# Kernel optimization log

Measured on AMD Instinct MI355X. Metric: run time of the kernel, lower is better.

## Reference

```python
import jax, jax.numpy as jnp
import numpy as np

B, S, D = 4, 8192, 1024

def log_g(x):
    # log of g(x): log(x + 0.5) for x >= 0, log(sigmoid(x)) = -softplus(-x) otherwise
    return jnp.where(x >= 0, jnp.log(jax.nn.relu(x) + 0.5), -jax.nn.softplus(-x))

def setup_inputs() -> dict:
    key = jax.random.key(0)
    k1, k2 = jax.random.split(key)
    x = jax.random.normal(k1, (B, S, D), dtype=jnp.float32)
    # Linear(dim, 3*dim, bias=False); stored as [dim, 3*dim] so y = x @ W
    W = jax.random.normal(k2, (D, 3 * D), dtype=jnp.float32) * (1.0 / np.sqrt(D))
    return {"x": x, "W": W}

def reference(x, W):
    # x: [B, S, D], W: [D, 3D]
    hW = jnp.einsum('bsd,de->bse', x, W)  # [B, S, 3D]
    hidden, f_gate, i_gate = jnp.split(hW, 3, axis=-1)

    # log-space normalized gates:
    # diff = softplus(-f) - softplus(-i); log_f' = -softplus(diff); log_i' = -softplus(-diff)
    diff = jax.nn.softplus(-f_gate) - jax.nn.softplus(-i_gate)
    log_f = -jax.nn.softplus(diff)
    log_i = -jax.nn.softplus(-diff)
    log_values = log_i + log_g(hidden)

    # Heinsen associative scan in log space (float32 internally)
    a_star = jnp.cumsum(log_f.astype(jnp.float32), axis=1)
    log_h0_plus_b_star = jax.lax.cumlogsumexp(log_values.astype(jnp.float32) - a_star, axis=1)
    log_h = a_star + log_h0_plus_b_star
    out = jnp.exp(log_h).astype(x.dtype)  # [B, S, D]
    return out
```

## Files before the change

### kernel.cpp

```cpp
#include <hip/hip_runtime.h>
#include <hip/hip_bf16.h>
#include <cstdint>
#include <cstddef>


#define BB 4
#define SS 8192
#define DD 1024
#define MM 32768
#define KK 1024
#define NN 3072
#define CHUNKS 256
#define CLEN 32
#define NCH 4096
#define NT 16

typedef __bf16 bf16;
typedef __bf16 bf16x2 __attribute__((ext_vector_type(2)));
typedef __bf16 bf16x4 __attribute__((ext_vector_type(4)));
typedef __bf16 bf16x8 __attribute__((ext_vector_type(8)));
typedef float f32x4 __attribute__((ext_vector_type(4)));

__device__ __forceinline__ void gload16(const bf16* g, bf16* l) {
  __builtin_amdgcn_global_load_lds(
      (const __attribute__((address_space(1))) unsigned int*)(const void*)g,
      (__attribute__((address_space(3))) unsigned int*)(void*)l,
      16, 0, 0);
}

__device__ __forceinline__ void gate2(float h, float f, float i,
                                      float& F, float& IG) {
  float P = __expf(fminf(-f, 80.f));
  float Q = __expf(fminf(-i, 80.f));
  float rZ = __builtin_amdgcn_rcpf(2.f + P + Q);
  float eh = __expf(fminf(-h, 80.f));
  float gh = (h >= 0.f) ? (h + 0.5f) : __builtin_amdgcn_rcpf(1.f + eh);
  F = (1.f + Q) * rZ;
  IG = (1.f + P) * gh * rZ;
}

__device__ __forceinline__ float laddexp(float a, float b) {
  float m = fmaxf(a, b);
  return m + __logf(1.f + __expf(fminf(a, b) - m));
}
__device__ __forceinline__ void comb(float& A, float& V, float Ac, float Vc) {
  V = laddexp(V + Ac, Vc);
  A += Ac;
}

__global__ __launch_bounds__(256) void k_cvt_x(const float4* __restrict__ x,
                                               bf16x4* __restrict__ xb) {
  int i = blockIdx.x * 256 + threadIdx.x;
  float4 v = x[i];
  bf16x4 o;
  o[0] = (bf16)v.x; o[1] = (bf16)v.y; o[2] = (bf16)v.z; o[3] = (bf16)v.w;
  xb[i] = o;
}

__global__ __launch_bounds__(256) void k_cvt_wt(const float* __restrict__ W,
                                                bf16* __restrict__ Wt) {
  __shared__ float tile[32][33];
  int n0 = blockIdx.x * 32, k0 = blockIdx.y * 32;
  int tx = threadIdx.x, ty = threadIdx.y;
#pragma unroll
  for (int i = 0; i < 32; i += 8)
    tile[ty + i][tx] = W[(size_t)(k0 + ty + i) * NN + n0 + tx];
  __syncthreads();
#pragma unroll
  for (int i = 0; i < 32; i += 8)
    Wt[(size_t)(n0 + ty + i) * KK + k0 + tx] = (bf16)tile[tx][ty + i];
}

__global__ __launch_bounds__(512, 2) void k_gemm(const bf16* __restrict__ A,
                                                 const bf16* __restrict__ Bt,
                                                 bf16* __restrict__ C) {
  __shared__ __align__(16) bf16 sm[65536];
  const int tid = threadIdx.x;
  const int lane = tid & 63;
  const int w = tid >> 6;
  const int wm = w >> 2;
  const int wn = w & 3;
  const int c16 = lane & 15;
  const int l4 = lane >> 4;

  int bid = blockIdx.x;
  int swz = (bid & 7) * 192 + (bid >> 3);
  int mT = swz / 12;
  int nT = swz - mT * 12;
  const int mBase = mT * 256, nBase = nT * 256;

  const int sr = tid >> 3;
  const int scol = ((tid & 7) ^ (sr & 7)) * 8;
  const bf16* gA = A + (size_t)(mBase + sr) * KK + scol;
  const bf16* gB = Bt + (size_t)(nBase + sr) * KK + scol;
  const int ld = tid * 8;

  const int sw8 = c16 & 7;
  const int sx0 = (l4 ^ sw8) * 8;
  const int sx1 = ((l4 + 4) ^ sw8) * 8;
  const int aRow = (wm * 64 + c16) * 64;
  const int bRow = (wn * 32 + c16) * 64;

  f32x4 acc[2][2][4][2];
#pragma unroll
  for (int a = 0; a < 2; ++a)
#pragma unroll
    for (int b2 = 0; b2 < 2; ++b2)
#pragma unroll
      for (int m = 0; m < 4; ++m)
#pragma unroll
        for (int n = 0; n < 2; ++n)
          acc[a][b2][m][n] = (f32x4){0.f, 0.f, 0.f, 0.f};

#define STGA(h, L, bo, ko) \
  gload16(gA + (h) * 131072 + (L) * 65536 + (ko), \
          sm + (bo) + (h) * 8192 + (L) * 4096 + ld)
#define STGB(h, L, bo, ko) \
  gload16(gB + (h) * 131072 + (L) * 65536 + (ko), \
          sm + (bo) + 16384 + (h) * 8192 + (L) * 4096 + ld)
#define LDA(qm, AF)                                                     \
  _Pragma("unroll") for (int mi = 0; mi < 4; ++mi) {                    \
    const bf16* p_ = sm + buf + (qm) * 8192 + aRow + mi * 1024;         \
    AF[mi][0] = *(const bf16x8*)(p_ + sx0);                             \
    AF[mi][1] = *(const bf16x8*)(p_ + sx1);                             \
  }
#define LDB(qn, BF)                                                     \
  _Pragma("unroll") for (int ni = 0; ni < 2; ++ni) {                    \
    const bf16* p_ = sm + buf + 16384 + (qn) * 8192 + bRow + ni * 1024; \
    BF[ni][0] = *(const bf16x8*)(p_ + sx0);                             \
    BF[ni][1] = *(const bf16x8*)(p_ + sx1);                             \
  }
#define MFMAQ(qm, qn, AF, BF)                                             \
  __builtin_amdgcn_s_setprio(1);                                          \
  _Pragma("unroll") for (int mi = 0; mi < 4; ++mi)                        \
  _Pragma("unroll") for (int ni = 0; ni < 2; ++ni) {                      \
    acc[qm][qn][mi][ni] = __builtin_amdgcn_mfma_f32_16x16x32_bf16(        \
        AF[mi][0], BF[ni][0], acc[qm][qn][mi][ni], 0, 0, 0);              \
    acc[qm][qn][mi][ni] = __builtin_amdgcn_mfma_f32_16x16x32_bf16(        \
        AF[mi][1], BF[ni][1], acc[qm][qn][mi][ni], 0, 0, 0);              \
  }                                                                       \
  __builtin_amdgcn_s_setprio(0);
#define BAR asm volatile("s_barrier" ::: "memory")
#define VMC(n) asm volatile("s_waitcnt vmcnt(" #n ")" ::: "memory")

  STGA(0, 0, 0, 0); STGA(0, 1, 0, 0); STGB(0, 0, 0, 0); STGB(0, 1, 0, 0);
  STGA(1, 0, 0, 0); STGA(1, 1, 0, 0); STGB(1, 0, 0, 0); STGB(1, 1, 0, 0);
  VMC(4);
  BAR;

  bf16x8 afr[4][2], bfr0[2][2], bfr1[2][2];

  for (int t = 0; t < NT - 1; ++t) {
    const int buf = (t & 1) << 15;
    const int nb = buf ^ 32768;
    const int ko = (t + 1) * 64;
    LDA(0, afr); LDB(0, bfr0);
    STGA(0, 0, nb, ko); STGA(0, 1, nb, ko);
    STGB(0, 0, nb, ko); STGB(0, 1, nb, ko);
    VMC(4);
    BAR;
    MFMAQ(0, 0, afr, bfr0);
    BAR;
    LDB(1, bfr1);
    STGA(1, 0, nb, ko); STGA(1, 1, nb, ko);
    BAR;
    MFMAQ(0, 1, afr, bfr1);
    BAR;
    LDA(1, afr);
    STGB(1, 0, nb, ko); STGB(1, 1, nb, ko);
    BAR;
    MFMAQ(1, 1, afr, bfr1);
    BAR;
    VMC(4);
    BAR;
    MFMAQ(1, 0, afr, bfr0);
    BAR;
  }
  {
    const int buf = 32768;
    LDA(0, afr); LDB(0, bfr0);
    VMC(0);
    BAR;
    MFMAQ(0, 0, afr, bfr0);
    BAR;
    LDB(1, bfr1);
    BAR;
    MFMAQ(0, 1, afr, bfr1);
    BAR;
    LDA(1, afr);
    BAR;
    MFMAQ(1, 1, afr, bfr1);
    BAR;
    MFMAQ(1, 0, afr, bfr0);
  }

  __syncthreads();
  const int rq = l4 * 4;
#pragma unroll
  for (int qm = 0; qm < 2; ++qm)
#pragma unroll
    for (int qn = 0; qn < 2; ++qn)
#pragma unroll
      for (int mi = 0; mi < 4; ++mi)
#pragma unroll
        for (int ni = 0; ni < 2; ++ni)
#pragma unroll
          for (int r = 0; r < 4; ++r) {
            int row = qm * 128 + wm * 64 + mi * 16 + rq + r;
            int col = (qn * 128 + wn * 32 + ni * 16 + c16) ^ ((row & 7) << 3);
            sm[row * 256 + col] = (bf16)acc[qm][qn][mi][ni][r];
          }
  __syncthreads();
#pragma unroll
  for (int p = 0; p < 16; ++p) {
    int row = p * 16 + (tid >> 5);
    int colL = (tid & 31) * 8;
    int col = colL ^ ((row & 7) << 3);
    bf16x8 v = *(const bf16x8*)(sm + row * 256 + col);
    *(bf16x8*)(C + (size_t)(mBase + row) * NN + nBase + colL) = v;
  }
#undef STGA
#undef STGB
#undef LDA
#undef LDB
#undef MFMAQ
#undef BAR
#undef VMC
}

__global__ __launch_bounds__(256, 6) void k_scan1(const bf16* __restrict__ hW,
                                                  float2* __restrict__ agg) {
  const int d0 = threadIdx.x * 4;
  const int b = blockIdx.y, c = blockIdx.z;
  const bf16* p = hW + (size_t)(b * SS + c * CLEN) * NN + d0;
  float Fp[4] = {1.f, 1.f, 1.f, 1.f};
  float v[4] = {0.f, 0.f, 0.f, 0.f};
  bf16x4 hh = *(const bf16x4*)(p);
  bf16x4 ff = *(const bf16x4*)(p + DD);
  bf16x4 ii = *(const bf16x4*)(p + 2 * DD);
#pragma unroll 4
  for (int j = 0; j < CLEN - 1; ++j) {
    p += NN;
    bf16x4 hn = *(const bf16x4*)(p);
    bf16x4 fn = *(const bf16x4*)(p + DD);
    bf16x4 in2 = *(const bf16x4*)(p + 2 * DD);
#pragma unroll
    for (int e = 0; e < 4; ++e) {
      float F, IG;
      gate2((float)hh[e], (float)ff[e], (float)ii[e], F, IG);
      v[e] = fmaf(v[e], F, IG);
      Fp[e] *= F;
    }
    hh = hn; ff = fn; ii = in2;
  }
#pragma unroll
  for (int e = 0; e < 4; ++e) {
    float F, IG;
    gate2((float)hh[e], (float)ff[e], (float)ii[e], F, IG);
    v[e] = fmaf(v[e], F, IG);
    Fp[e] *= F;
  }
  const size_t ch = (size_t)b * DD + d0;
#pragma unroll
  for (int e = 0; e < 4; ++e)
    agg[(ch + e) * CHUNKS + c] =
        make_float2(__logf(fmaxf(Fp[e], 1e-37f)), __logf(fmaxf(v[e], 1e-37f)));
}

__global__ __launch_bounds__(256) void k_scan2(const float2* __restrict__ agg,
                                               float2* __restrict__ pre) {
  const int ch = blockIdx.x * 4 + (threadIdx.x >> 6);
  const int lane = threadIdx.x & 63;
  const float4* src = (const float4*)(agg + (size_t)ch * CHUNKS);
  float4 v0 = src[lane * 2];
  float4 v1 = src[lane * 2 + 1];
  float A = v0.x, V = v0.y;
  comb(A, V, v0.z, v0.w);
  comb(A, V, v1.x, v1.y);
  comb(A, V, v1.z, v1.w);
#pragma unroll
  for (int off = 1; off < 64; off <<= 1) {
    float Ao = __shfl_up(A, off);
    float Vo = __shfl_up(V, off);
    if (lane >= off) {
      V = laddexp(Vo + A, V);
      A = Ao + A;
    }
  }
  float exA = __shfl_up(A, 1);
  float exV = __shfl_up(V, 1);
  if (lane == 0) { exA = 0.f; exV = -1e30f; }
  float4 o0, o1;
  o0.x = exA; o0.y = exV;
  comb(exA, exV, v0.x, v0.y);
  o0.z = exA; o0.w = exV;
  comb(exA, exV, v0.z, v0.w);
  o1.x = exA; o1.y = exV;
  comb(exA, exV, v1.x, v1.y);
  o1.z = exA; o1.w = exV;
  float4* dst = (float4*)(pre + (size_t)ch * CHUNKS);
  dst[lane * 2] = o0;
  dst[lane * 2 + 1] = o1;
}

__global__ __launch_bounds__(256, 6) void k_scan3(const bf16* __restrict__ hW,
                                                  const float2* __restrict__ pre,
                                                  float* __restrict__ out) {
  const int d0 = threadIdx.x * 4;
  const int b = blockIdx.y, c = blockIdx.z;
  const bf16* p = hW + (size_t)(b * SS + c * CLEN) * NN + d0;
  float* o = out + (size_t)(b * SS + c * CLEN) * DD + d0;
  const size_t ch = (size_t)b * DD + d0;
  float v[4];
#pragma unroll
  for (int e = 0; e < 4; ++e)
    v[e] = __expf(pre[(ch + e) * CHUNKS + c].y);
  bf16x4 hh = *(const bf16x4*)(p);
  bf16x4 ff = *(const bf16x4*)(p + DD);
  bf16x4 ii = *(const bf16x4*)(p + 2 * DD);
#pragma unroll 4
  for (int j = 0; j < CLEN - 1; ++j) {
    p += NN;
    bf16x4 hn = *(const bf16x4*)(p);
    bf16x4 fn = *(const bf16x4*)(p + DD);
    bf16x4 in2 = *(const bf16x4*)(p + 2 * DD);
    float4 ov;
#pragma unroll
    for (int e = 0; e < 4; ++e) {
      float F, IG;
      gate2((float)hh[e], (float)ff[e], (float)ii[e], F, IG);
      v[e] = fmaf(v[e], F, IG);
    }
    ov.x = v[0]; ov.y = v[1]; ov.z = v[2]; ov.w = v[3];
    *(float4*)o = ov;
    o += DD;
    hh = hn; ff = fn; ii = in2;
  }
  float4 ov;
#pragma unroll
  for (int e = 0; e < 4; ++e) {
    float F, IG;
    gate2((float)hh[e], (float)ff[e], (float)ii[e], F, IG);
    v[e] = fmaf(v[e], F, IG);
  }
  ov.x = v[0]; ov.y = v[1]; ov.z = v[2]; ov.w = v[3];
  *(float4*)o = ov;
}

extern "C" void kernel_launch(void* const* d_in, const int* in_sizes, int n_in,
                              void* d_out, int out_size, void* d_ws,
                              size_t ws_size, hipStream_t stream) {
  const float* x = (const float*)d_in[0];
  const float* W = (const float*)d_in[1];
  float* out = (float*)d_out;
  char* ws = (char*)d_ws;

  const size_t wtB = (size_t)NN * KK * 2;
  const size_t xbB = (size_t)MM * KK * 2;
  const size_t aggB = (size_t)CHUNKS * NCH * sizeof(float2);
  bf16* Wt = (bf16*)ws;
  bf16* xb = (bf16*)(ws + wtB);
  bf16* hW = (bf16*)(ws + wtB + xbB);
  float2* agg = (float2*)(ws + wtB);
  float2* pre = (float2*)(ws + wtB + aggB);

  k_cvt_wt<<<dim3(NN / 32, KK / 32), dim3(32, 8), 0, stream>>>(W, Wt);
  k_cvt_x<<<dim3(MM * KK / 4 / 256), dim3(256), 0, stream>>>((const float4*)x,
                                                             (bf16x4*)xb);
  k_gemm<<<dim3((NN / 256) * (MM / 256)), 512, 0, stream>>>(xb, Wt, hW);
  k_scan1<<<dim3(1, BB, CHUNKS), 256, 0, stream>>>(hW, agg);
  k_scan2<<<dim3(NCH / 4), 256, 0, stream>>>(agg, pre);
  k_scan3<<<dim3(1, BB, CHUNKS), 256, 0, stream>>>(hW, pre, out);
}
```

Before: 533.6 us.

## Remove GEMM inner barriers, use exp2 gates, prefetch two rows in scans

Several barriers are removed between the MFMA and LDS-load phases of the GEMM main loop. The gate math now uses hardware exp2 with prescaled arguments. The scan kernels drop the occupancy hint from launch bounds and keep two rows of prefetched loads in flight instead of one. This aims to cut synchronisation stalls and hide memory latency, but the barrier removal risks LDS read/write races between the double-buffered stages.

```diff
diff --git a/kernel.cpp b/kernel.cpp
--- a/kernel.cpp
+++ b/kernel.cpp
@@ -28,13 +28,20 @@
       16, 0, 0);
 }
 
+#if __has_builtin(__builtin_amdgcn_exp2f)
+#define EXP2(x) __builtin_amdgcn_exp2f(x)
+#else
+#define EXP2(x) __expf((x) * 0.69314718056f)
+#endif
+
 __device__ __forceinline__ void gate2(float h, float f, float i,
                                       float& F, float& IG) {
-  float P = __expf(fminf(-f, 80.f));
-  float Q = __expf(fminf(-i, 80.f));
+  const float NL2E = -1.44269504089f;
+  float P = EXP2(fminf(f * NL2E, 60.f));
+  float Q = EXP2(fminf(i * NL2E, 60.f));
+  float H = EXP2(fminf(h * NL2E, 60.f));
   float rZ = __builtin_amdgcn_rcpf(2.f + P + Q);
-  float eh = __expf(fminf(-h, 80.f));
-  float gh = (h >= 0.f) ? (h + 0.5f) : __builtin_amdgcn_rcpf(1.f + eh);
+  float gh = (h >= 0.f) ? (h + 0.5f) : __builtin_amdgcn_rcpf(1.f + H);
   F = (1.f + Q) * rZ;
   IG = (1.f + P) * gh * rZ;
 }
@@ -160,21 +167,15 @@
     VMC(4);
     BAR;
     MFMAQ(0, 0, afr, bfr0);
-    BAR;
     LDB(1, bfr1);
     STGA(1, 0, nb, ko); STGA(1, 1, nb, ko);
-    BAR;
     MFMAQ(0, 1, afr, bfr1);
-    BAR;
     LDA(1, afr);
     STGB(1, 0, nb, ko); STGB(1, 1, nb, ko);
-    BAR;
     MFMAQ(1, 1, afr, bfr1);
-    BAR;
     VMC(4);
     BAR;
     MFMAQ(1, 0, afr, bfr0);
-    BAR;
   }
   {
     const int buf = 32768;
@@ -182,15 +183,10 @@
     VMC(0);
     BAR;
     MFMAQ(0, 0, afr, bfr0);
-    BAR;
     LDB(1, bfr1);
-    BAR;
     MFMAQ(0, 1, afr, bfr1);
-    BAR;
     LDA(1, afr);
-    BAR;
     MFMAQ(1, 1, afr, bfr1);
-    BAR;
     MFMAQ(1, 0, afr, bfr0);
   }
 
@@ -228,35 +224,48 @@
 #undef VMC
 }
 
-__global__ __launch_bounds__(256, 6) void k_scan1(const bf16* __restrict__ hW,
-                                                  float2* __restrict__ agg) {
+__global__ __launch_bounds__(256) void k_scan1(const bf16* __restrict__ hW,
+                                               float2* __restrict__ agg) {
   const int d0 = threadIdx.x * 4;
   const int b = blockIdx.y, c = blockIdx.z;
   const bf16* p = hW + (size_t)(b * SS + c * CLEN) * NN + d0;
   float Fp[4] = {1.f, 1.f, 1.f, 1.f};
   float v[4] = {0.f, 0.f, 0.f, 0.f};
-  bf16x4 hh = *(const bf16x4*)(p);
-  bf16x4 ff = *(const bf16x4*)(p + DD);
-  bf16x4 ii = *(const bf16x4*)(p + 2 * DD);
-#pragma unroll 4
-  for (int j = 0; j < CLEN - 1; ++j) {
-    p += NN;
+  bf16x4 hA = *(const bf16x4*)(p);
+  bf16x4 fA = *(const bf16x4*)(p + DD);
+  bf16x4 iA = *(const bf16x4*)(p + 2 * DD);
+  const bf16* p1 = p + NN;
+  bf16x4 hB = *(const bf16x4*)(p1);
+  bf16x4 fB = *(const bf16x4*)(p1 + DD);
+  bf16x4 iB = *(const bf16x4*)(p1 + 2 * DD);
+  p += 2 * NN;
+#pragma unroll 2
+  for (int j = 0; j < CLEN - 2; ++j) {
     bf16x4 hn = *(const bf16x4*)(p);
     bf16x4 fn = *(const bf16x4*)(p + DD);
     bf16x4 in2 = *(const bf16x4*)(p + 2 * DD);
+    p += NN;
 #pragma unroll
     for (int e = 0; e < 4; ++e) {
       float F, IG;
-      gate2((float)hh[e], (float)ff[e], (float)ii[e], F, IG);
+      gate2((float)hA[e], (float)fA[e], (float)iA[e], F, IG);
       v[e] = fmaf(v[e], F, IG);
       Fp[e] *= F;
     }
-    hh = hn; ff = fn; ii = in2;
+    hA = hB; fA = fB; iA = iB;
+    hB = hn; fB = fn; iB = in2;
   }
 #pragma unroll
   for (int e = 0; e < 4; ++e) {
     float F, IG;
-    gate2((float)hh[e], (float)ff[e], (float)ii[e], F, IG);
+    gate2((float)hA[e], (float)fA[e], (float)iA[e], F, IG);
+    v[e] = fmaf(v[e], F, IG);
+    Fp[e] *= F;
+  }
+#pragma unroll
+  for (int e = 0; e < 4; ++e) {
+    float F, IG;
+    gate2((float)hB[e], (float)fB[e], (float)iB[e], F, IG);
     v[e] = fmaf(v[e], F, IG);
     Fp[e] *= F;
   }
@@ -303,9 +312,9 @@
   dst[lane * 2 + 1] = o1;
 }
 
-__global__ __launch_bounds__(256, 6) void k_scan3(const bf16* __restrict__ hW,
-                                                  const float2* __restrict__ pre,
-                                                  float* __restrict__ out) {
+__global__ __launch_bounds__(256) void k_scan3(const bf16* __restrict__ hW,
+                                               const float2* __restrict__ pre,
+                                               float* __restrict__ out) {
   const int d0 = threadIdx.x * 4;
   const int b = blockIdx.y, c = blockIdx.z;
   const bf16* p = hW + (size_t)(b * SS + c * CLEN) * NN + d0;
@@ -315,36 +324,56 @@
 #pragma unroll
   for (int e = 0; e < 4; ++e)
     v[e] = __expf(pre[(ch + e) * CHUNKS + c].y);
-  bf16x4 hh = *(const bf16x4*)(p);
-  bf16x4 ff = *(const bf16x4*)(p + DD);
-  bf16x4 ii = *(const bf16x4*)(p + 2 * DD);
-#pragma unroll 4
-  for (int j = 0; j < CLEN - 1; ++j) {
-    p += NN;
+  bf16x4 hA = *(const bf16x4*)(p);
+  bf16x4 fA = *(const bf16x4*)(p + DD);
+  bf16x4 iA = *(const bf16x4*)(p + 2 * DD);
+  const bf16* p1 = p + NN;
+  bf16x4 hB = *(const bf16x4*)(p1);
+  bf16x4 fB = *(const bf16x4*)(p1 + DD);
+  bf16x4 iB = *(const bf16x4*)(p1 + 2 * DD);
+  p += 2 * NN;
+#pragma unroll 2
+  for (int j = 0; j < CLEN - 2; ++j) {
     bf16x4 hn = *(const bf16x4*)(p);
     bf16x4 fn = *(const bf16x4*)(p + DD);
     bf16x4 in2 = *(const bf16x4*)(p + 2 * DD);
+    p += NN;
     float4 ov;
 #pragma unroll
     for (int e = 0; e < 4; ++e) {
       float F, IG;
-      gate2((float)hh[e], (float)ff[e], (float)ii[e], F, IG);
+      gate2((float)hA[e], (float)fA[e], (float)iA[e], F, IG);
       v[e] = fmaf(v[e], F, IG);
     }
     ov.x = v[0]; ov.y = v[1]; ov.z = v[2]; ov.w = v[3];
     *(float4*)o = ov;
     o += DD;
-    hh = hn; ff = fn; ii = in2;
-  }
-  float4 ov;
-#pragma unroll
-  for (int e = 0; e < 4; ++e) {
-    float F, IG;
-    gate2((float)hh[e], (float)ff[e], (float)ii[e], F, IG);
-    v[e] = fmaf(v[e], F, IG);
-  }
-  ov.x = v[0]; ov.y = v[1]; ov.z = v[2]; ov.w = v[3];
-  *(float4*)o = ov;
+    hA = hB; fA = fB; iA = iB;
+    hB = hn; fB = fn; iB = in2;
+  }
+  {
+    float4 ov;
+#pragma unroll
+    for (int e = 0; e < 4; ++e) {
+      float F, IG;
+      gate2((float)hA[e], (float)fA[e], (float)iA[e], F, IG);
+      v[e] = fmaf(v[e], F, IG);
+    }
+    ov.x = v[0]; ov.y = v[1]; ov.z = v[2]; ov.w = v[3];
+    *(float4*)o = ov;
+    o += DD;
+  }
+  {
+    float4 ov;
+#pragma unroll
+    for (int e = 0; e < 4; ++e) {
+      float F, IG;
+      gate2((float)hB[e], (float)fB[e], (float)iB[e], F, IG);
+      v[e] = fmaf(v[e], F, IG);
+    }
+    ov.x = v[0]; ov.y = v[1]; ov.z = v[2]; ov.w = v[3];
+    *(float4*)o = ov;
+  }
 }
 
 extern "C" void kernel_launch(void* const* d_in, const int* in_sizes, int n_in,
```

After: 528.2 us. No clear change (-1.0%).
